# Kernel tuning notes

Hardware: AMD Instinct MI355X
Metric: run time of the kernel (lower is better)

## Reference

```python
import jax, jax.numpy as jnp
import numpy as np

ALPHA = 0.9

def setup_inputs() -> dict:
    key = jax.random.key(0)
    inputs = jax.random.normal(key, (16, 4000, 512), dtype=jnp.float32)
    return {"inputs": inputs}

def reference(inputs) -> jnp.ndarray:
    # y_t = (1-alpha) * y_{t-1} + alpha * x_t, with y_{-1} = 0
    # (matches torch loop: y_0 = alpha * x_0)
    a = jnp.asarray(ALPHA, dtype=inputs.dtype)
    one_minus_a = jnp.asarray(1.0 - ALPHA, dtype=inputs.dtype)
    x_t = jnp.swapaxes(inputs, 0, 1)  # [T, B, C] for scan over time

    def step(carry, x):
        y = one_minus_a * carry + a * x
        return y, y

    init = jnp.zeros(x_t.shape[1:], dtype=inputs.dtype)  # [B, C]
    _, ys = jax.lax.scan(step, init, x_t)  # ys: [T, B, C]
    return jnp.swapaxes(ys, 0, 1)  # [B, T, C]
```

## Files before the change

kernel.cpp:

```cpp
#include <hip/hip_runtime.h>


constexpr int B_ = 16;
constexpr int T_ = 4000;
constexpr int C_ = 512;
constexpr int L_ = 20;
constexpr int W_ = 8;
constexpr int NC4_ = C_ / 4;
constexpr int NCHUNK_ = T_ / L_;
constexpr int BATCH_ = 10;

__global__ __launch_bounds__(256, 8) void ema_chunk_scan(const float* __restrict__ x,
                                                         float* __restrict__ y) {
    int g = blockIdx.x * blockDim.x + threadIdx.x;
    int c4 = g & (NC4_ - 1);
    int bt = g >> 7;
    int b  = bt & (B_ - 1);
    int chunk = bt >> 4;

    int t0 = chunk * L_;
    const float a = 0.9f, om = 0.1f;
    float4 acc = make_float4(0.f, 0.f, 0.f, 0.f);

    if (chunk > 0) {
        const float4* pw = (const float4*)(x + ((size_t)b * T_ + (t0 - W_)) * C_) + c4;
        float4 wbuf[W_];
        #pragma unroll
        for (int i = 0; i < W_; ++i) wbuf[i] = pw[(size_t)i * NC4_];
        #pragma unroll
        for (int i = 0; i < W_; ++i) {
            acc.x = om * acc.x + a * wbuf[i].x;
            acc.y = om * acc.y + a * wbuf[i].y;
            acc.z = om * acc.z + a * wbuf[i].z;
            acc.w = om * acc.w + a * wbuf[i].w;
        }
    }

    const float4* pm = (const float4*)(x + ((size_t)b * T_ + t0) * C_) + c4;
    float4*       q  = (float4*)(y + ((size_t)b * T_ + t0) * C_) + c4;
    #pragma unroll
    for (int blk = 0; blk < L_ / BATCH_; ++blk) {
        float4 buf[BATCH_];
        #pragma unroll
        for (int i = 0; i < BATCH_; ++i) buf[i] = pm[(size_t)i * NC4_];
        pm += (size_t)BATCH_ * NC4_;
        #pragma unroll
        for (int i = 0; i < BATCH_; ++i) {
            acc.x = om * acc.x + a * buf[i].x;
            acc.y = om * acc.y + a * buf[i].y;
            acc.z = om * acc.z + a * buf[i].z;
            acc.w = om * acc.w + a * buf[i].w;
            buf[i] = acc;
        }
        #pragma unroll
        for (int i = 0; i < BATCH_; ++i) q[(size_t)i * NC4_] = buf[i];
        q += (size_t)BATCH_ * NC4_;
    }
}

extern "C" void kernel_launch(void* const* d_in, const int* in_sizes, int n_in,
                              void* d_out, int out_size, void* d_ws, size_t ws_size,
                              hipStream_t stream) {
    const float* x = (const float*)d_in[0];
    float* y = (float*)d_out;
    int total_threads = B_ * NC4_ * NCHUNK_;
    int block = 256;
    int grid = total_threads / block;
    ema_chunk_scan<<<grid, block, 0, stream>>>(x, y);
}
```

Before: 236.9 us.

## Shrink time chunks and issue all halo and chunk loads up front

Result: faster. 228.6 us (-3.5%).

```diff
diff --git a/kernel.cpp b/kernel.cpp
--- a/kernel.cpp
+++ b/kernel.cpp
@@ -4,13 +4,12 @@
 constexpr int B_ = 16;
 constexpr int T_ = 4000;
 constexpr int C_ = 512;
-constexpr int L_ = 20;
+constexpr int L_ = 8;
 constexpr int W_ = 8;
 constexpr int NC4_ = C_ / 4;
 constexpr int NCHUNK_ = T_ / L_;
-constexpr int BATCH_ = 10;
 
-__global__ __launch_bounds__(256, 8) void ema_chunk_scan(const float* __restrict__ x,
+__global__ __launch_bounds__(256, 4) void ema_chunk_scan(const float* __restrict__ x,
                                                          float* __restrict__ y) {
     int g = blockIdx.x * blockDim.x + threadIdx.x;
     int c4 = g & (NC4_ - 1);
@@ -19,42 +18,39 @@
     int chunk = bt >> 4;
 
     int t0 = chunk * L_;
+    int tw = (chunk > 0) ? (t0 - W_) : 0;
+
+    const float4* pw = (const float4*)(x + ((size_t)b * T_ + tw) * C_) + c4;
+    const float4* pm = (const float4*)(x + ((size_t)b * T_ + t0) * C_) + c4;
+    float4*       q  = (float4*)(y + ((size_t)b * T_ + t0) * C_) + c4;
+
+    float4 w[W_];
+    #pragma unroll
+    for (int i = 0; i < W_; ++i) w[i] = pw[(size_t)i * NC4_];
+    float4 m[L_];
+    #pragma unroll
+    for (int i = 0; i < L_; ++i) m[i] = pm[(size_t)i * NC4_];
+
     const float a = 0.9f, om = 0.1f;
     float4 acc = make_float4(0.f, 0.f, 0.f, 0.f);
 
-    if (chunk > 0) {
-        const float4* pw = (const float4*)(x + ((size_t)b * T_ + (t0 - W_)) * C_) + c4;
-        float4 wbuf[W_];
-        #pragma unroll
-        for (int i = 0; i < W_; ++i) wbuf[i] = pw[(size_t)i * NC4_];
-        #pragma unroll
-        for (int i = 0; i < W_; ++i) {
-            acc.x = om * acc.x + a * wbuf[i].x;
-            acc.y = om * acc.y + a * wbuf[i].y;
-            acc.z = om * acc.z + a * wbuf[i].z;
-            acc.w = om * acc.w + a * wbuf[i].w;
-        }
+    #pragma unroll
+    for (int i = 0; i < W_; ++i) {
+        acc.x = om * acc.x + a * w[i].x;
+        acc.y = om * acc.y + a * w[i].y;
+        acc.z = om * acc.z + a * w[i].z;
+        acc.w = om * acc.w + a * w[i].w;
     }
+    float sel = (chunk > 0) ? 1.f : 0.f;
+    acc.x *= sel; acc.y *= sel; acc.z *= sel; acc.w *= sel;
 
-    const float4* pm = (const float4*)(x + ((size_t)b * T_ + t0) * C_) + c4;
-    float4*       q  = (float4*)(y + ((size_t)b * T_ + t0) * C_) + c4;
     #pragma unroll
-    for (int blk = 0; blk < L_ / BATCH_; ++blk) {
-        float4 buf[BATCH_];
-        #pragma unroll
-        for (int i = 0; i < BATCH_; ++i) buf[i] = pm[(size_t)i * NC4_];
-        pm += (size_t)BATCH_ * NC4_;
-        #pragma unroll
-        for (int i = 0; i < BATCH_; ++i) {
-            acc.x = om * acc.x + a * buf[i].x;
-            acc.y = om * acc.y + a * buf[i].y;
-            acc.z = om * acc.z + a * buf[i].z;
-            acc.w = om * acc.w + a * buf[i].w;
-            buf[i] = acc;
-        }
-        #pragma unroll
-        for (int i = 0; i < BATCH_; ++i) q[(size_t)i * NC4_] = buf[i];
-        q += (size_t)BATCH_ * NC4_;
+    for (int i = 0; i < L_; ++i) {
+        acc.x = om * acc.x + a * m[i].x;
+        acc.y = om * acc.y + a * m[i].y;
+        acc.z = om * acc.z + a * m[i].z;
+        acc.w = om * acc.w + a * m[i].w;
+        q[(size_t)i * NC4_] = acc;
     }
 }
 
```
